# Kernel tuning notes

Hardware: AMD Instinct MI355X
Metric: run time of the kernel (lower is better)

## Reference

```python
import jax, jax.numpy as jnp
import numpy as np

N = 64      # features
L = 96      # history length
LP = 24     # prediction length
H = 128     # rnn hidden
B = 1024    # batch


def setup_inputs() -> dict:
    key = jax.random.key(0)
    ks = jax.random.split(key, 16)
    # monotonically increasing timestamps
    tp_all = jnp.cumsum(jax.random.uniform(ks[0], (B, L + LP), dtype=jnp.float32), axis=1)
    tp_true = tp_all[:, :L]
    tp_pred = tp_all[:, L:]
    X = jax.random.normal(ks[1], (B, L, N), dtype=jnp.float32)
    mask = jax.random.randint(ks[2], (B, L, N), 0, 2).astype(jnp.float32)
    def unif(k, shape, fan):
        std = 1.0 / np.sqrt(fan)
        return jax.random.uniform(k, shape, jnp.float32, -std, std)
    # TemporalDecay for h: W (H,N), b (H); std = 1/sqrt(out)
    Wh_dec = unif(ks[3], (H, N), H)
    bh_dec = unif(ks[4], (H,), H)
    # TemporalDecay for x (diag): W (N,N) but only diagonal used
    Wx_dec = unif(ks[5], (N, N), N)
    bx_dec = unif(ks[6], (N,), N)
    # GRUCell: input size = 2N + H
    in_sz = 2 * N + H
    W_ih = unif(ks[7], (3 * H, in_sz), H)
    W_hh = unif(ks[8], (3 * H, H), H)
    b_ih = unif(ks[9], (3 * H,), H)
    b_hh = unif(ks[10], (3 * H,), H)
    # output projection
    Wp = unif(ks[11], (N, H), H)
    bp = unif(ks[12], (N,), H)
    return {"tp_pred": tp_pred, "X": X, "tp_true": tp_true, "mask": mask,
            "Wh_dec": Wh_dec, "bh_dec": bh_dec, "Wx_dec": Wx_dec, "bx_dec": bx_dec,
            "W_ih": W_ih, "W_hh": W_hh, "b_ih": b_ih, "b_hh": b_hh,
            "Wp": Wp, "bp": bp}


def _grud(tp_pred, X, tp_true, mask, Wh_dec, bh_dec, Wx_dec, bx_dec,
          W_ih, W_hh, b_ih, b_hh, Wp, bp):
    Bsz, Lh, Nf = X.shape
    Lp = tp_pred.shape[1]
    Lall = Lh + Lp
    Hh = Wh_dec.shape[0]

    # pad future with zeros (unobserved)
    X_all = jnp.concatenate([X, jnp.zeros((Bsz, Lp, Nf), X.dtype)], axis=1)
    M_all = jnp.concatenate([mask, jnp.zeros((Bsz, Lp, Nf), X.dtype)], axis=1)
    tp = jnp.concatenate([tp_true, tp_pred], axis=1)

    # deltas: first-difference padded with 0 at t=0, broadcast over features
    dt = jnp.pad(tp[:, 1:] - tp[:, :-1], ((0, 0), (1, 0)))  # (B, Lall)
    deltas = jnp.broadcast_to(dt[:, :, None], (Bsz, Lall, Nf))

    # empirical mean over positions where (1 - mask) == 1 (faithful to source)
    valid = 1.0 - M_all
    cnt = jnp.clip(valid.sum(axis=1), 1.0, None)  # (B, N)
    mu = (X_all * valid).sum(axis=1) / cnt        # (B, N)

    # LOCF as in source: where mask != 0, copy previous value
    def locf_step(prev, xm):
        x_t, m_t = xm
        cur = jnp.where(m_t != 0, prev, x_t)
        return cur, cur
    _, X_locf = jax.lax.scan(locf_step, X_all[:, 0],
                             (jnp.swapaxes(X_all, 0, 1), jnp.swapaxes(M_all, 0, 1)))
    # X_locf: (Lall, B, N)

    diag_Wx = jnp.diag(Wx_dec)  # (N,) -- diag=True masks W with identity

    def step(h, inputs):
        x_t, m_t, d_t, xl_t = inputs  # each (B, N)
        gh = jnp.exp(-jax.nn.relu(d_t @ Wh_dec.T + bh_dec))      # (B, H)
        gx = jnp.exp(-jax.nn.relu(d_t * diag_Wx + bx_dec))       # (B, N)
        h = h * gh
        rep = h
        x_h = gx * xl_t + (1.0 - gx) * mu
        x_in = m_t * x_t + (1.0 - m_t) * x_h
        inp = jnp.concatenate([x_in, h, m_t], axis=1)             # (B, 2N+H)
        gi = inp @ W_ih.T + b_ih                                  # (B, 3H)
        gr = h @ W_hh.T + b_hh                                    # (B, 3H)
        r = jax.nn.sigmoid(gi[:, :Hh] + gr[:, :Hh])
        z = jax.nn.sigmoid(gi[:, Hh:2 * Hh] + gr[:, Hh:2 * Hh])
        n = jnp.tanh(gi[:, 2 * Hh:] + r * gr[:, 2 * Hh:])
        h_new = (1.0 - z) * n + z * h
        return h_new, rep

    h0 = jnp.zeros((Bsz, Hh), X.dtype)
    xs = (jnp.swapaxes(X_all, 0, 1), jnp.swapaxes(M_all, 0, 1),
          jnp.swapaxes(deltas, 0, 1), X_locf)
    _, reps = jax.lax.scan(step, h0, xs)          # (Lall, B, H)
    reps = jnp.swapaxes(reps, 0, 1)               # (B, Lall, H)
    recon = reps @ Wp.T + bp                      # (B, Lall, N)
    y_hat = recon[:, -Lp:]                        # (B, Lp, N)
    return y_hat[None]                            # (1, B, Lp, N)


def reference(tp_pred, X, tp_true, mask, Wh_dec, bh_dec, Wx_dec, bx_dec,
              W_ih, W_hh, b_ih, b_hh, Wp, bp):
    return _grud(tp_pred, X, tp_true, mask, Wh_dec, bh_dec, Wx_dec, bx_dec,
                 W_ih, W_hh, b_ih, b_hh, Wp, bp)
```

## Files before the change

### kernel.cpp

```cpp
#include <hip/hip_runtime.h>

#define L2E 1.4426950408889634f

typedef _Float16 f16x8 __attribute__((ext_vector_type(8)));
typedef _Float16 f16x4 __attribute__((ext_vector_type(4)));
typedef float f32x4 __attribute__((ext_vector_type(4)));

__device__ __forceinline__ float sig_fast(float x) {
    return __builtin_amdgcn_rcpf(1.0f + __builtin_amdgcn_exp2f(-L2E * x));
}
__device__ __forceinline__ float tanh_fast(float x) {
    return 1.0f - 2.0f * __builtin_amdgcn_rcpf(1.0f + __builtin_amdgcn_exp2f(2.0f * L2E * x));
}
__device__ __forceinline__ float expnr_fast(float x) {
    return __builtin_amdgcn_exp2f(-L2E * fmaxf(x, 0.0f));
}
__device__ __forceinline__ void barrier_lds_only() {
    __asm__ volatile("s_waitcnt lgkmcnt(0)\n\ts_barrier" ::: "memory");
}

struct F8 { float v[8]; };
__device__ __forceinline__ F8 ld8(const float* p) {
    F8 r;
    float4 a = *(const float4*)p, b = *(const float4*)(p + 4);
    r.v[0]=a.x; r.v[1]=a.y; r.v[2]=a.z; r.v[3]=a.w;
    r.v[4]=b.x; r.v[5]=b.y; r.v[6]=b.z; r.v[7]=b.w;
    return r;
}
__device__ __forceinline__ f16x8 cvt8(F8 a) {
    f16x8 r;
#pragma unroll
    for (int q = 0; q < 8; ++q) r[q] = (_Float16)a.v[q];
    return r;
}
__device__ __forceinline__ f16x8 cvt8s(F8 a, F8 b) {
    f16x8 r;
#pragma unroll
    for (int q = 0; q < 8; ++q) r[q] = (_Float16)(a.v[q] + b.v[q]);
    return r;
}

__global__ __launch_bounds__(512, 2) void grud_kernel(
    const float* __restrict__ tp_pred, const float* __restrict__ X,
    const float* __restrict__ tp_true, const float* __restrict__ mask,
    const float* __restrict__ Wh_dec, const float* __restrict__ bh_dec,
    const float* __restrict__ Wx_dec, const float* __restrict__ bx_dec,
    const float* __restrict__ W_ih, const float* __restrict__ W_hh,
    const float* __restrict__ b_ih, const float* __restrict__ b_hh,
    const float* __restrict__ Wp, const float* __restrict__ bp,
    float* __restrict__ out)
{
    constexpr int SR = 136;
    __shared__ alignas(16) _Float16 ring[8 * 2048];
    __shared__ alignas(16) _Float16 V[2][16 * SR];
    __shared__ alignas(16) _Float16 Astage[16 * SR];
    __shared__ float dt_lds[480];
    __shared__ float mu_l[4][64];
    __shared__ float wxl[64], bxl[64];
    __shared__ char occ_pad[34000];

    const int tid  = threadIdx.x;
    const int w    = tid >> 6, l = tid & 63, quad = l >> 4, lm = l & 15;
    const int b0   = blockIdx.x * 4;

    if (tid > 100000) occ_pad[0] = 1;

    for (int i = tid; i < 16 * SR; i += 512) ((unsigned*)V)[i] = 0;

    if (tid < 480) {
        int t = tid >> 2, q = tid & 3, b = b0 + q;
        float v = 0.0f;
        if (t) {
            float cur = (t < 96) ? tp_true[b * 96 + t] : tp_pred[b * 24 + t - 96];
            float prv = (t - 1 < 96) ? tp_true[b * 96 + t - 1] : tp_pred[b * 24 + t - 97];
            v = cur - prv;
        }
        dt_lds[tid] = v;
    }
    if (tid < 64) { wxl[tid] = Wx_dec[tid * 65]; bxl[tid] = bx_dec[tid]; }

    if (w >= 4) {
        const int pw   = w - 4;
        const int ptid = tid - 256;
        const int c0   = 32 * pw + lm, c1 = c0 + 16;

        {
            const float* xr = X    + ((size_t)(b0 + pw) * 96) * 64 + l;
            const float* mr = mask + ((size_t)(b0 + pw) * 96) * 64 + l;
            float a = 0.0f, c = 0.0f;
#pragma unroll 4
            for (int t = 0; t < 96; ++t) {
                float x = xr[t * 64], m = mr[t * 64];
                a += x * (1.0f - m); c += 1.0f - m;
            }
            mu_l[pw][l] = a / (c + 24.0f);
        }

        f16x8 wxf[3][2][4];
#pragma unroll
        for (int g = 0; g < 3; ++g)
#pragma unroll
            for (int j = 0; j < 2; ++j)
#pragma unroll
                for (int fi = 0; fi < 4; ++fi) {
                    const int row = g * 128 + (j ? c1 : c0);
                    const int k0 = fi * 32 + quad * 8;
                    wxf[g][j][fi] = cvt8(ld8(W_ih + row * 256 + (k0 < 64 ? k0 : 128 + k0)));
                }

        const int pn = pw * 16 + lm;
        const float bpv = bp[pn];
        f16x8 wPf[4];
#pragma unroll
        for (int fi = 0; fi < 4; ++fi)
            wPf[fi] = cvt8(ld8(Wp + pn * 128 + fi * 32 + quad * 8));

        auto prodLoad = [&](int gp, float4& px, float4& pm) {
            if (gp >= 24) { px = make_float4(0,0,0,0); pm = make_float4(0,0,0,0); return; }
            const int R = ptid >> 4, tg = 4 * gp + (R >> 2), b = R & 3;
            const size_t o = (((size_t)(b0 + b) * 96) + tg) * 64 + (ptid & 15) * 4;
            px = *(const float4*)(X + o);
            pm = *(const float4*)(mask + o);
        };
        auto prodStage = [&](int gp, float4 px, float4 pm) {
            const int R = ptid >> 4, toff = R >> 2, b = R & 3;
            const int tg = 4 * gp + toff, n0 = (ptid & 15) * 4;
            const float d = dt_lds[tg * 4 + b];
            const float xs[4] = {px.x, px.y, px.z, px.w};
            const float ms[4] = {pm.x, pm.y, pm.z, pm.w};
            f16x4 xi, mm;
#pragma unroll
            for (int e = 0; e < 4; ++e) {
                const int n = n0 + e;
                const float gxv = expnr_fast(d * wxl[n] + bxl[n]);
                const float muv = mu_l[b][n];
                float v;
                if (gp < 24) {
                    v = (ms[e] != 0.0f) ? xs[e] : (xs[e] - muv) * gxv + muv;
                    mm[e] = (_Float16)ms[e];
                } else {
                    v = (1.0f - gxv) * muv;
                    mm[e] = (_Float16)0.0f;
                }
                xi[e] = (_Float16)v;
            }
            *(f16x4*)&Astage[R * SR + n0]      = xi;
            *(f16x4*)&Astage[R * SR + 64 + n0] = mm;
        };
        auto prodMMA = [&](int gp, int j) {
            f16x8 ap[4];
#pragma unroll
            for (int fi = 0; fi < 4; ++fi)
                ap[fi] = *(const f16x8*)&Astage[lm * SR + fi * 32 + quad * 8];
            const int c = j ? c1 : c0;
            const int slot = (4 * gp + quad) & 7;
            f32x4 aR = {0,0,0,0}, aZ = {0,0,0,0}, aN = {0,0,0,0};
#pragma unroll
            for (int fi = 0; fi < 4; ++fi) {
                aR = __builtin_amdgcn_mfma_f32_16x16x32_f16(ap[fi], wxf[0][j][fi], aR, 0, 0, 0);
                aZ = __builtin_amdgcn_mfma_f32_16x16x32_f16(ap[fi], wxf[1][j][fi], aZ, 0, 0, 0);
                aN = __builtin_amdgcn_mfma_f32_16x16x32_f16(ap[fi], wxf[2][j][fi], aN, 0, 0, 0);
            }
#pragma unroll
            for (int rb = 0; rb < 4; ++rb) {
                f16x4 pk = {(_Float16)aR[rb], (_Float16)aZ[rb], (_Float16)aN[rb], (_Float16)0.0f};
                *(f16x4*)&ring[slot * 2048 + c * 16 + rb * 4] = pk;
            }
        };

        __syncthreads();
        {
            float4 px, pm;
            prodLoad(0, px, pm);
            prodStage(0, px, pm);
            prodMMA(0, 0); prodMMA(0, 1);
        }
        __syncthreads();

        float4 px, pm;
        for (int t = 0; t < 120; ++t) {
            const int gp = (t >> 2) + 1, ph = t & 3;
            if (ph == 0)      { if (gp < 30) prodLoad(gp, px, pm); }
            else if (ph == 1) { if (gp < 30) prodStage(gp, px, pm); }
            else if (ph == 2) { if (gp < 30) prodMMA(gp, 0); }
            else              { if (gp < 30) prodMMA(gp, 1); }

            if (t >= 96) {
                f16x8 af[4];
#pragma unroll
                for (int fi = 0; fi < 4; ++fi)
                    af[fi] = *(const f16x8*)&V[t & 1][lm * SR + fi * 32 + quad * 8];
                f32x4 aP = {bpv, 0, 0, 0};
#pragma unroll
                for (int fi = 0; fi < 4; ++fi)
                    aP = __builtin_amdgcn_mfma_f32_16x16x32_f16(af[fi], wPf[fi], aP, 0, 0, 0);
                out[((size_t)(b0 + quad) * 24 + (t - 96)) * 64 + pn] = aP[0];
            }
            barrier_lds_only();
        }
    } else {
        const int c0 = 32 * w + lm, c1 = c0 + 16;

        f16x8 wR[2][4], wZ[2][4], wN[2][4], wG[2][4];
        float S_[2], bh_[2], bR_[2], bZ_[2], bN_[2], bG_[2];
#pragma unroll
        for (int j = 0; j < 2; ++j) {
            const int c = j ? c1 : c0;
#pragma unroll
            for (int fi = 0; fi < 4; ++fi) {
                const int k0 = fi * 32 + quad * 8;
                wR[j][fi] = cvt8s(ld8(W_ih + c * 256 + 64 + k0),
                                  ld8(W_hh + c * 128 + k0));
                wZ[j][fi] = cvt8s(ld8(W_ih + (128 + c) * 256 + 64 + k0),
                                  ld8(W_hh + (128 + c) * 128 + k0));
                wN[j][fi] = cvt8(ld8(W_ih + (256 + c) * 256 + 64 + k0));
                wG[j][fi] = cvt8(ld8(W_hh + (256 + c) * 128 + k0));
            }
            float s = 0.0f;
            const float4* wh4 = (const float4*)(Wh_dec + c * 64);
#pragma unroll
            for (int i = 0; i < 16; ++i) { float4 u = wh4[i]; s += u.x + u.y + u.z + u.w; }
            S_[j]  = s;
            bh_[j] = bh_dec[c];
            bR_[j] = b_ih[c] + b_hh[c];
            bZ_[j] = b_ih[128 + c] + b_hh[128 + c];
            bN_[j] = b_ih[256 + c];
            bG_[j] = b_hh[256 + c];
        }

        __syncthreads();
        __syncthreads();

        float h0 = 0.0f, h1 = 0.0f;
        for (int t = 0; t < 120; ++t) {
            const _Float16* Vp = V[t & 1];
            const int sb = (t & 7) * 2048;
            const f16x4 g0 = *(const f16x4*)&ring[sb + c0 * 16 + quad * 4];
            const f16x4 g1 = *(const f16x4*)&ring[sb + c1 * 16 + quad * 4];
            f16x8 af[4];
#pragma unroll
            for (int fi = 0; fi < 4; ++fi)
                af[fi] = *(const f16x8*)&Vp[lm * SR + fi * 32 + quad * 8];

            f32x4 aR0 = {(float)g0[0] + bR_[0], 0, 0, 0};
            f32x4 aZ0 = {(float)g0[1] + bZ_[0], 0, 0, 0};
            f32x4 aN0 = {(float)g0[2] + bN_[0], 0, 0, 0};
            f32x4 aG0 = {bG_[0], 0, 0, 0};
            f32x4 aR1 = {(float)g1[0] + bR_[1], 0, 0, 0};
            f32x4 aZ1 = {(float)g1[1] + bZ_[1], 0, 0, 0};
            f32x4 aN1 = {(float)g1[2] + bN_[1], 0, 0, 0};
            f32x4 aG1 = {bG_[1], 0, 0, 0};
#pragma unroll
            for (int fi = 0; fi < 4; ++fi) {
                aR0 = __builtin_amdgcn_mfma_f32_16x16x32_f16(af[fi], wR[0][fi], aR0, 0, 0, 0);
                aZ0 = __builtin_amdgcn_mfma_f32_16x16x32_f16(af[fi], wZ[0][fi], aZ0, 0, 0, 0);
                aN0 = __builtin_amdgcn_mfma_f32_16x16x32_f16(af[fi], wN[0][fi], aN0, 0, 0, 0);
                aG0 = __builtin_amdgcn_mfma_f32_16x16x32_f16(af[fi], wG[0][fi], aG0, 0, 0, 0);
                aR1 = __builtin_amdgcn_mfma_f32_16x16x32_f16(af[fi], wR[1][fi], aR1, 0, 0, 0);
                aZ1 = __builtin_amdgcn_mfma_f32_16x16x32_f16(af[fi], wZ[1][fi], aZ1, 0, 0, 0);
                aN1 = __builtin_amdgcn_mfma_f32_16x16x32_f16(af[fi], wN[1][fi], aN1, 0, 0, 0);
                aG1 = __builtin_amdgcn_mfma_f32_16x16x32_f16(af[fi], wG[1][fi], aG1, 0, 0, 0);
            }

            {
                const float rg0 = sig_fast(aR0[0]), zg0 = sig_fast(aZ0[0]);
                const float ng0 = tanh_fast(aN0[0] + rg0 * aG0[0]);
                h0 = zg0 * (h0 - ng0) + ng0;
                const float rg1 = sig_fast(aR1[0]), zg1 = sig_fast(aZ1[0]);
                const float ng1 = tanh_fast(aN1[0] + rg1 * aG1[0]);
                h1 = zg1 * (h1 - ng1) + ng1;
            }
            if (t < 119) {
                const float d = dt_lds[(t + 1) * 4 + quad];
                h0 *= expnr_fast(d * S_[0] + bh_[0]);
                h1 *= expnr_fast(d * S_[1] + bh_[1]);
                _Float16* Vn = V[(t & 1) ^ 1];
                Vn[(4 * quad) * SR + c0] = (_Float16)h0;
                Vn[(4 * quad) * SR + c1] = (_Float16)h1;
            }
            barrier_lds_only();
        }
    }
}

extern "C" void kernel_launch(void* const* d_in, const int* in_sizes, int n_in,
                              void* d_out, int out_size, void* d_ws, size_t ws_size,
                              hipStream_t stream) {
    const float* tp_pred = (const float*)d_in[0];
    const float* X       = (const float*)d_in[1];
    const float* tp_true = (const float*)d_in[2];
    const float* mask    = (const float*)d_in[3];
    const float* Wh_dec  = (const float*)d_in[4];
    const float* bh_dec  = (const float*)d_in[5];
    const float* Wx_dec  = (const float*)d_in[6];
    const float* bx_dec  = (const float*)d_in[7];
    const float* W_ih    = (const float*)d_in[8];
    const float* W_hh    = (const float*)d_in[9];
    const float* b_ih    = (const float*)d_in[10];
    const float* b_hh    = (const float*)d_in[11];
    const float* Wp      = (const float*)d_in[12];
    const float* bp      = (const float*)d_in[13];

    grud_kernel<<<dim3(256), dim3(512), 0, stream>>>(
        tp_pred, X, tp_true, mask, Wh_dec, bh_dec, Wx_dec, bx_dec,
        W_ih, W_hh, b_ih, b_hh, Wp, bp, (float*)d_out);
}
```

Baseline: 204.1 us.

## Split recurrent hidden columns across eight consumer waves with 768-thread blocks

Blocks grow from 512 to 768 threads: eight consumer waves each own 16 hidden columns instead of four waves owning 32, while the four producer waves stay. The LDS occupancy padding is removed and launch bounds change to 768 threads with 3 blocks per CU. The per-step time decay is computed before the MFMAs so it overlaps, and the precomputed input gate terms are added after the matrix products, not as the accumulator seed. This shortens the serial per-step critical path per wave at the cost of more waves per block and different occupancy and barrier behaviour.

```diff
diff --git a/kernel.cpp b/kernel.cpp
--- a/kernel.cpp
+++ b/kernel.cpp
@@ -40,7 +40,7 @@
     return r;
 }
 
-__global__ __launch_bounds__(512, 2) void grud_kernel(
+__global__ __launch_bounds__(768, 3) void grud_kernel(
     const float* __restrict__ tp_pred, const float* __restrict__ X,
     const float* __restrict__ tp_true, const float* __restrict__ mask,
     const float* __restrict__ Wh_dec, const float* __restrict__ bh_dec,
@@ -57,15 +57,12 @@
     __shared__ float dt_lds[480];
     __shared__ float mu_l[4][64];
     __shared__ float wxl[64], bxl[64];
-    __shared__ char occ_pad[34000];
 
     const int tid  = threadIdx.x;
     const int w    = tid >> 6, l = tid & 63, quad = l >> 4, lm = l & 15;
     const int b0   = blockIdx.x * 4;
 
-    if (tid > 100000) occ_pad[0] = 1;
-
-    for (int i = tid; i < 16 * SR; i += 512) ((unsigned*)V)[i] = 0;
+    for (int i = tid; i < 16 * SR; i += 768) ((unsigned*)V)[i] = 0;
 
     if (tid < 480) {
         int t = tid >> 2, q = tid & 3, b = b0 + q;
@@ -79,9 +76,9 @@
     }
     if (tid < 64) { wxl[tid] = Wx_dec[tid * 65]; bxl[tid] = bx_dec[tid]; }
 
-    if (w >= 4) {
-        const int pw   = w - 4;
-        const int ptid = tid - 256;
+    if (w >= 8) {
+        const int pw   = w - 8;
+        const int ptid = tid - 512;
         const int c0   = 32 * pw + lm, c1 = c0 + 16;
 
         {
@@ -173,9 +170,10 @@
             float4 px, pm;
             prodLoad(0, px, pm);
             prodStage(0, px, pm);
+            barrier_lds_only();
             prodMMA(0, 0); prodMMA(0, 1);
-        }
-        __syncthreads();
+            barrier_lds_only();
+        }
 
         float4 px, pm;
         for (int t = 0; t < 120; ++t) {
@@ -199,85 +197,66 @@
             barrier_lds_only();
         }
     } else {
-        const int c0 = 32 * w + lm, c1 = c0 + 16;
-
-        f16x8 wR[2][4], wZ[2][4], wN[2][4], wG[2][4];
-        float S_[2], bh_[2], bR_[2], bZ_[2], bN_[2], bG_[2];
-#pragma unroll
-        for (int j = 0; j < 2; ++j) {
-            const int c = j ? c1 : c0;
-#pragma unroll
-            for (int fi = 0; fi < 4; ++fi) {
-                const int k0 = fi * 32 + quad * 8;
-                wR[j][fi] = cvt8s(ld8(W_ih + c * 256 + 64 + k0),
-                                  ld8(W_hh + c * 128 + k0));
-                wZ[j][fi] = cvt8s(ld8(W_ih + (128 + c) * 256 + 64 + k0),
-                                  ld8(W_hh + (128 + c) * 128 + k0));
-                wN[j][fi] = cvt8(ld8(W_ih + (256 + c) * 256 + 64 + k0));
-                wG[j][fi] = cvt8(ld8(W_hh + (256 + c) * 128 + k0));
-            }
-            float s = 0.0f;
+        const int c = 16 * w + lm;
+
+        f16x8 wR[4], wZ[4], wN[4], wG[4];
+#pragma unroll
+        for (int fi = 0; fi < 4; ++fi) {
+            const int k0 = fi * 32 + quad * 8;
+            wR[fi] = cvt8s(ld8(W_ih + c * 256 + 64 + k0),
+                           ld8(W_hh + c * 128 + k0));
+            wZ[fi] = cvt8s(ld8(W_ih + (128 + c) * 256 + 64 + k0),
+                           ld8(W_hh + (128 + c) * 128 + k0));
+            wN[fi] = cvt8(ld8(W_ih + (256 + c) * 256 + 64 + k0));
+            wG[fi] = cvt8(ld8(W_hh + (256 + c) * 128 + k0));
+        }
+        float S = 0.0f;
+        {
             const float4* wh4 = (const float4*)(Wh_dec + c * 64);
 #pragma unroll
-            for (int i = 0; i < 16; ++i) { float4 u = wh4[i]; s += u.x + u.y + u.z + u.w; }
-            S_[j]  = s;
-            bh_[j] = bh_dec[c];
-            bR_[j] = b_ih[c] + b_hh[c];
-            bZ_[j] = b_ih[128 + c] + b_hh[128 + c];
-            bN_[j] = b_ih[256 + c];
-            bG_[j] = b_hh[256 + c];
-        }
+            for (int i = 0; i < 16; ++i) { float4 u = wh4[i]; S += u.x + u.y + u.z + u.w; }
+        }
+        const float bhc = bh_dec[c];
+        const float bRc = b_ih[c] + b_hh[c];
+        const float bZc = b_ih[128 + c] + b_hh[128 + c];
+        const float bNc = b_ih[256 + c];
+        const float bGc = b_hh[256 + c];
 
         __syncthreads();
-        __syncthreads();
-
-        float h0 = 0.0f, h1 = 0.0f;
+        barrier_lds_only();
+        barrier_lds_only();
+
+        const f32x4 ZV = {0.0f, 0.0f, 0.0f, 0.0f};
+        float h = 0.0f;
         for (int t = 0; t < 120; ++t) {
             const _Float16* Vp = V[t & 1];
-            const int sb = (t & 7) * 2048;
-            const f16x4 g0 = *(const f16x4*)&ring[sb + c0 * 16 + quad * 4];
-            const f16x4 g1 = *(const f16x4*)&ring[sb + c1 * 16 + quad * 4];
+            const f16x4 g = *(const f16x4*)&ring[(t & 7) * 2048 + c * 16 + quad * 4];
             f16x8 af[4];
 #pragma unroll
             for (int fi = 0; fi < 4; ++fi)
                 af[fi] = *(const f16x8*)&Vp[lm * SR + fi * 32 + quad * 8];
 
-            f32x4 aR0 = {(float)g0[0] + bR_[0], 0, 0, 0};
-            f32x4 aZ0 = {(float)g0[1] + bZ_[0], 0, 0, 0};
-            f32x4 aN0 = {(float)g0[2] + bN_[0], 0, 0, 0};
-            f32x4 aG0 = {bG_[0], 0, 0, 0};
-            f32x4 aR1 = {(float)g1[0] + bR_[1], 0, 0, 0};
-            f32x4 aZ1 = {(float)g1[1] + bZ_[1], 0, 0, 0};
-            f32x4 aN1 = {(float)g1[2] + bN_[1], 0, 0, 0};
-            f32x4 aG1 = {bG_[1], 0, 0, 0};
-#pragma unroll
-            for (int fi = 0; fi < 4; ++fi) {
-                aR0 = __builtin_amdgcn_mfma_f32_16x16x32_f16(af[fi], wR[0][fi], aR0, 0, 0, 0);
-                aZ0 = __builtin_amdgcn_mfma_f32_16x16x32_f16(af[fi], wZ[0][fi], aZ0, 0, 0, 0);
-                aN0 = __builtin_amdgcn_mfma_f32_16x16x32_f16(af[fi], wN[0][fi], aN0, 0, 0, 0);
-                aG0 = __builtin_amdgcn_mfma_f32_16x16x32_f16(af[fi], wG[0][fi], aG0, 0, 0, 0);
-                aR1 = __builtin_amdgcn_mfma_f32_16x16x32_f16(af[fi], wR[1][fi], aR1, 0, 0, 0);
-                aZ1 = __builtin_amdgcn_mfma_f32_16x16x32_f16(af[fi], wZ[1][fi], aZ1, 0, 0, 0);
-                aN1 = __builtin_amdgcn_mfma_f32_16x16x32_f16(af[fi], wN[1][fi], aN1, 0, 0, 0);
-                aG1 = __builtin_amdgcn_mfma_f32_16x16x32_f16(af[fi], wG[1][fi], aG1, 0, 0, 0);
-            }
-
-            {
-                const float rg0 = sig_fast(aR0[0]), zg0 = sig_fast(aZ0[0]);
-                const float ng0 = tanh_fast(aN0[0] + rg0 * aG0[0]);
-                h0 = zg0 * (h0 - ng0) + ng0;
-                const float rg1 = sig_fast(aR1[0]), zg1 = sig_fast(aZ1[0]);
-                const float ng1 = tanh_fast(aN1[0] + rg1 * aG1[0]);
-                h1 = zg1 * (h1 - ng1) + ng1;
-            }
-            if (t < 119) {
-                const float d = dt_lds[(t + 1) * 4 + quad];
-                h0 *= expnr_fast(d * S_[0] + bh_[0]);
-                h1 *= expnr_fast(d * S_[1] + bh_[1]);
-                _Float16* Vn = V[(t & 1) ^ 1];
-                Vn[(4 * quad) * SR + c0] = (_Float16)h0;
-                Vn[(4 * quad) * SR + c1] = (_Float16)h1;
-            }
+            const int tn = (t < 119) ? t + 1 : 119;
+            const float ghd = expnr_fast(dt_lds[tn * 4 + quad] * S + bhc);
+
+            f32x4 aR = __builtin_amdgcn_mfma_f32_16x16x32_f16(af[0], wR[0], ZV, 0, 0, 0);
+            f32x4 aZ = __builtin_amdgcn_mfma_f32_16x16x32_f16(af[0], wZ[0], ZV, 0, 0, 0);
+            f32x4 aN = __builtin_amdgcn_mfma_f32_16x16x32_f16(af[0], wN[0], ZV, 0, 0, 0);
+            f32x4 aG = __builtin_amdgcn_mfma_f32_16x16x32_f16(af[0], wG[0], ZV, 0, 0, 0);
+#pragma unroll
+            for (int fi = 1; fi < 4; ++fi) {
+                aR = __builtin_amdgcn_mfma_f32_16x16x32_f16(af[fi], wR[fi], aR, 0, 0, 0);
+                aZ = __builtin_amdgcn_mfma_f32_16x16x32_f16(af[fi], wZ[fi], aZ, 0, 0, 0);
+                aN = __builtin_amdgcn_mfma_f32_16x16x32_f16(af[fi], wN[fi], aN, 0, 0, 0);
+                aG = __builtin_amdgcn_mfma_f32_16x16x32_f16(af[fi], wG[fi], aG, 0, 0, 0);
+            }
+
+            const float rg = sig_fast(aR[0] + ((float)g[0] + bRc));
+            const float zg = sig_fast(aZ[0] + ((float)g[1] + bZc));
+            const float ng = tanh_fast(aN[0] + ((float)g[2] + bNc) + rg * (aG[0] + bGc));
+            h = (zg * (h - ng) + ng) * ghd;
+            if (t < 119)
+                V[(t & 1) ^ 1][(4 * quad) * SR + c] = (_Float16)h;
             barrier_lds_only();
         }
     }
@@ -301,7 +280,7 @@
     const float* Wp      = (const float*)d_in[12];
     const float* bp      = (const float*)d_in[13];
 
-    grud_kernel<<<dim3(256), dim3(512), 0, stream>>>(
+    grud_kernel<<<dim3(256), dim3(768), 0, stream>>>(
         tp_pred, X, tp_true, mask, Wh_dec, bh_dec, Wx_dec, bx_dec,
         W_ih, W_hh, b_ih, b_hh, Wp, bp, (float*)d_out);
 }
```

Result: slower. 209.8 us (+2.8%).

## Compact hidden-state LDS buffer, re-layout ring, merge producer MMAs, hoist decay

Applied to the files above, without the earlier changes.

Shrinks the hidden-state double buffer from 16 padded rows to 4 rows, with lanes addressing rows by lm>>2, and changes the ring layout to row-major with a padded stride. It also merges the producer's two per-column MMA phases into one and moves the temporal-decay exponential ahead of the MFMA chain. The recurrent MFMAs now start from zero accumulators, with biases added afterwards. The occupancy padding array is removed, which raises LDS-limited occupancy, and the extra __syncthreads are replaced with LDS-only barriers. These changes aim to cut LDS traffic and footprint and shorten the serial critical path per timestep. The risk is that the reordered bias addition changes precision slightly.

```diff
diff --git a/kernel.cpp b/kernel.cpp
--- a/kernel.cpp
+++ b/kernel.cpp
@@ -50,25 +50,24 @@
     const float* __restrict__ Wp, const float* __restrict__ bp,
     float* __restrict__ out)
 {
-    constexpr int SR = 136;
-    __shared__ alignas(16) _Float16 ring[8 * 2048];
-    __shared__ alignas(16) _Float16 V[2][16 * SR];
-    __shared__ alignas(16) _Float16 Astage[16 * SR];
+    constexpr int VR = 136;
+    constexpr int AR = 136;
+    constexpr int RS = 2056;
+    __shared__ alignas(16) _Float16 ring[8 * RS];
+    __shared__ alignas(16) _Float16 V4[2][4 * VR];
+    __shared__ alignas(16) _Float16 Astage[16 * AR];
     __shared__ float dt_lds[480];
     __shared__ float mu_l[4][64];
     __shared__ float wxl[64], bxl[64];
-    __shared__ char occ_pad[34000];
 
     const int tid  = threadIdx.x;
     const int w    = tid >> 6, l = tid & 63, quad = l >> 4, lm = l & 15;
     const int b0   = blockIdx.x * 4;
 
-    if (tid > 100000) occ_pad[0] = 1;
-
-    for (int i = tid; i < 16 * SR; i += 512) ((unsigned*)V)[i] = 0;
+    for (int i = tid; i < 4 * VR; i += 512) ((unsigned*)V4)[i] = 0;
 
     if (tid < 480) {
-        int t = tid >> 2, q = tid & 3, b = b0 + q;
+        int t = tid >> 2, b = b0 + (tid & 3);
         float v = 0.0f;
         if (t) {
             float cur = (t < 96) ? tp_true[b * 96 + t] : tp_pred[b * 24 + t - 96];
@@ -144,27 +143,32 @@
                 }
                 xi[e] = (_Float16)v;
             }
-            *(f16x4*)&Astage[R * SR + n0]      = xi;
-            *(f16x4*)&Astage[R * SR + 64 + n0] = mm;
+            *(f16x4*)&Astage[R * AR + n0]      = xi;
+            *(f16x4*)&Astage[R * AR + 64 + n0] = mm;
         };
-        auto prodMMA = [&](int gp, int j) {
+        auto prodMMA = [&](int gp) {
             f16x8 ap[4];
 #pragma unroll
             for (int fi = 0; fi < 4; ++fi)
-                ap[fi] = *(const f16x8*)&Astage[lm * SR + fi * 32 + quad * 8];
-            const int c = j ? c1 : c0;
+                ap[fi] = *(const f16x8*)&Astage[lm * AR + fi * 32 + quad * 8];
             const int slot = (4 * gp + quad) & 7;
-            f32x4 aR = {0,0,0,0}, aZ = {0,0,0,0}, aN = {0,0,0,0};
+            f32x4 aR0 = {0,0,0,0}, aZ0 = {0,0,0,0}, aN0 = {0,0,0,0};
+            f32x4 aR1 = {0,0,0,0}, aZ1 = {0,0,0,0}, aN1 = {0,0,0,0};
 #pragma unroll
             for (int fi = 0; fi < 4; ++fi) {
-                aR = __builtin_amdgcn_mfma_f32_16x16x32_f16(ap[fi], wxf[0][j][fi], aR, 0, 0, 0);
-                aZ = __builtin_amdgcn_mfma_f32_16x16x32_f16(ap[fi], wxf[1][j][fi], aZ, 0, 0, 0);
-                aN = __builtin_amdgcn_mfma_f32_16x16x32_f16(ap[fi], wxf[2][j][fi], aN, 0, 0, 0);
+                aR0 = __builtin_amdgcn_mfma_f32_16x16x32_f16(ap[fi], wxf[0][0][fi], aR0, 0, 0, 0);
+                aZ0 = __builtin_amdgcn_mfma_f32_16x16x32_f16(ap[fi], wxf[1][0][fi], aZ0, 0, 0, 0);
+                aN0 = __builtin_amdgcn_mfma_f32_16x16x32_f16(ap[fi], wxf[2][0][fi], aN0, 0, 0, 0);
+                aR1 = __builtin_amdgcn_mfma_f32_16x16x32_f16(ap[fi], wxf[0][1][fi], aR1, 0, 0, 0);
+                aZ1 = __builtin_amdgcn_mfma_f32_16x16x32_f16(ap[fi], wxf[1][1][fi], aZ1, 0, 0, 0);
+                aN1 = __builtin_amdgcn_mfma_f32_16x16x32_f16(ap[fi], wxf[2][1][fi], aN1, 0, 0, 0);
             }
 #pragma unroll
             for (int rb = 0; rb < 4; ++rb) {
-                f16x4 pk = {(_Float16)aR[rb], (_Float16)aZ[rb], (_Float16)aN[rb], (_Float16)0.0f};
-                *(f16x4*)&ring[slot * 2048 + c * 16 + rb * 4] = pk;
+                f16x4 p0 = {(_Float16)aR0[rb], (_Float16)aZ0[rb], (_Float16)aN0[rb], (_Float16)0.0f};
+                f16x4 p1 = {(_Float16)aR1[rb], (_Float16)aZ1[rb], (_Float16)aN1[rb], (_Float16)0.0f};
+                *(f16x4*)&ring[slot * RS + (rb * 128 + c0) * 4] = p0;
+                *(f16x4*)&ring[slot * RS + (rb * 128 + c1) * 4] = p1;
             }
         };
 
@@ -173,23 +177,24 @@
             float4 px, pm;
             prodLoad(0, px, pm);
             prodStage(0, px, pm);
-            prodMMA(0, 0); prodMMA(0, 1);
-        }
-        __syncthreads();
-
+            barrier_lds_only();
+            prodMMA(0);
+            barrier_lds_only();
+        }
+
+        const int prow = (lm >> 2) * VR + quad * 8;
         float4 px, pm;
         for (int t = 0; t < 120; ++t) {
             const int gp = (t >> 2) + 1, ph = t & 3;
             if (ph == 0)      { if (gp < 30) prodLoad(gp, px, pm); }
             else if (ph == 1) { if (gp < 30) prodStage(gp, px, pm); }
-            else if (ph == 2) { if (gp < 30) prodMMA(gp, 0); }
-            else              { if (gp < 30) prodMMA(gp, 1); }
+            else if (ph == 2) { if (gp < 30) prodMMA(gp); }
 
             if (t >= 96) {
                 f16x8 af[4];
 #pragma unroll
                 for (int fi = 0; fi < 4; ++fi)
-                    af[fi] = *(const f16x8*)&V[t & 1][lm * SR + fi * 32 + quad * 8];
+                    af[fi] = *(const f16x8*)&V4[t & 1][prow + fi * 32];
                 f32x4 aP = {bpv, 0, 0, 0};
 #pragma unroll
                 for (int fi = 0; fi < 4; ++fi)
@@ -229,29 +234,37 @@
         }
 
         __syncthreads();
-        __syncthreads();
-
+        barrier_lds_only();
+        barrier_lds_only();
+
+        const f32x4 ZV = {0.0f, 0.0f, 0.0f, 0.0f};
+        const int vrow = (lm >> 2) * VR + quad * 8;
         float h0 = 0.0f, h1 = 0.0f;
         for (int t = 0; t < 120; ++t) {
-            const _Float16* Vp = V[t & 1];
-            const int sb = (t & 7) * 2048;
-            const f16x4 g0 = *(const f16x4*)&ring[sb + c0 * 16 + quad * 4];
-            const f16x4 g1 = *(const f16x4*)&ring[sb + c1 * 16 + quad * 4];
+            const _Float16* Vp = V4[t & 1];
+            const int sb = (t & 7) * RS + quad * 512;
+            const f16x4 g0 = *(const f16x4*)&ring[sb + c0 * 4];
+            const f16x4 g1 = *(const f16x4*)&ring[sb + c1 * 4];
             f16x8 af[4];
 #pragma unroll
             for (int fi = 0; fi < 4; ++fi)
-                af[fi] = *(const f16x8*)&Vp[lm * SR + fi * 32 + quad * 8];
-
-            f32x4 aR0 = {(float)g0[0] + bR_[0], 0, 0, 0};
-            f32x4 aZ0 = {(float)g0[1] + bZ_[0], 0, 0, 0};
-            f32x4 aN0 = {(float)g0[2] + bN_[0], 0, 0, 0};
-            f32x4 aG0 = {bG_[0], 0, 0, 0};
-            f32x4 aR1 = {(float)g1[0] + bR_[1], 0, 0, 0};
-            f32x4 aZ1 = {(float)g1[1] + bZ_[1], 0, 0, 0};
-            f32x4 aN1 = {(float)g1[2] + bN_[1], 0, 0, 0};
-            f32x4 aG1 = {bG_[1], 0, 0, 0};
-#pragma unroll
-            for (int fi = 0; fi < 4; ++fi) {
+                af[fi] = *(const f16x8*)&Vp[vrow + fi * 32];
+
+            const int tn = (t < 119) ? t + 1 : 119;
+            const float dn = dt_lds[tn * 4 + quad];
+            const float ghd0 = expnr_fast(dn * S_[0] + bh_[0]);
+            const float ghd1 = expnr_fast(dn * S_[1] + bh_[1]);
+
+            f32x4 aR0 = __builtin_amdgcn_mfma_f32_16x16x32_f16(af[0], wR[0][0], ZV, 0, 0, 0);
+            f32x4 aZ0 = __builtin_amdgcn_mfma_f32_16x16x32_f16(af[0], wZ[0][0], ZV, 0, 0, 0);
+            f32x4 aN0 = __builtin_amdgcn_mfma_f32_16x16x32_f16(af[0], wN[0][0], ZV, 0, 0, 0);
+            f32x4 aG0 = __builtin_amdgcn_mfma_f32_16x16x32_f16(af[0], wG[0][0], ZV, 0, 0, 0);
+            f32x4 aR1 = __builtin_amdgcn_mfma_f32_16x16x32_f16(af[0], wR[1][0], ZV, 0, 0, 0);
+            f32x4 aZ1 = __builtin_amdgcn_mfma_f32_16x16x32_f16(af[0], wZ[1][0], ZV, 0, 0, 0);
+            f32x4 aN1 = __builtin_amdgcn_mfma_f32_16x16x32_f16(af[0], wN[1][0], ZV, 0, 0, 0);
+            f32x4 aG1 = __builtin_amdgcn_mfma_f32_16x16x32_f16(af[0], wG[1][0], ZV, 0, 0, 0);
+#pragma unroll
+            for (int fi = 1; fi < 4; ++fi) {
                 aR0 = __builtin_amdgcn_mfma_f32_16x16x32_f16(af[fi], wR[0][fi], aR0, 0, 0, 0);
                 aZ0 = __builtin_amdgcn_mfma_f32_16x16x32_f16(af[fi], wZ[0][fi], aZ0, 0, 0, 0);
                 aN0 = __builtin_amdgcn_mfma_f32_16x16x32_f16(af[fi], wN[0][fi], aN0, 0, 0, 0);
@@ -262,21 +275,18 @@
                 aG1 = __builtin_amdgcn_mfma_f32_16x16x32_f16(af[fi], wG[1][fi], aG1, 0, 0, 0);
             }
 
-            {
-                const float rg0 = sig_fast(aR0[0]), zg0 = sig_fast(aZ0[0]);
-                const float ng0 = tanh_fast(aN0[0] + rg0 * aG0[0]);
-                h0 = zg0 * (h0 - ng0) + ng0;
-                const float rg1 = sig_fast(aR1[0]), zg1 = sig_fast(aZ1[0]);
-                const float ng1 = tanh_fast(aN1[0] + rg1 * aG1[0]);
-                h1 = zg1 * (h1 - ng1) + ng1;
-            }
+            const float rg0 = sig_fast(aR0[0] + ((float)g0[0] + bR_[0]));
+            const float zg0 = sig_fast(aZ0[0] + ((float)g0[1] + bZ_[0]));
+            const float ng0 = tanh_fast(aN0[0] + ((float)g0[2] + bN_[0]) + rg0 * (aG0[0] + bG_[0]));
+            h0 = (zg0 * (h0 - ng0) + ng0) * ghd0;
+            const float rg1 = sig_fast(aR1[0] + ((float)g1[0] + bR_[1]));
+            const float zg1 = sig_fast(aZ1[0] + ((float)g1[1] + bZ_[1]));
+            const float ng1 = tanh_fast(aN1[0] + ((float)g1[2] + bN_[1]) + rg1 * (aG1[0] + bG_[1]));
+            h1 = (zg1 * (h1 - ng1) + ng1) * ghd1;
             if (t < 119) {
-                const float d = dt_lds[(t + 1) * 4 + quad];
-                h0 *= expnr_fast(d * S_[0] + bh_[0]);
-                h1 *= expnr_fast(d * S_[1] + bh_[1]);
-                _Float16* Vn = V[(t & 1) ^ 1];
-                Vn[(4 * quad) * SR + c0] = (_Float16)h0;
-                Vn[(4 * quad) * SR + c1] = (_Float16)h1;
+                _Float16* Vn = V4[(t & 1) ^ 1];
+                Vn[quad * VR + c0] = (_Float16)h0;
+                Vn[quad * VR + c1] = (_Float16)h1;
             }
             barrier_lds_only();
         }
```

New measurement: 199.0 us. 2.5% less time.
